# Kernel optimization log

Measured on AMD Instinct MI355X. Metric: run time of the kernel, lower is better.

## Reference

```python
import jax, jax.numpy as jnp
import numpy as np

VOCAB, H, B, L = 32000, 1024, 64, 256  # L leaves per complete binary tree


def setup_inputs() -> dict:
    key = jax.random.key(0)
    ks = jax.random.split(key, 12)
    s = 1.0 / np.sqrt(H)
    return {
        "tokens": jax.random.randint(ks[0], (B, L), 0, VOCAB),
        "emb":    jax.random.normal(ks[1], (VOCAB, H), jnp.float32) * 0.02,
        "W_iock": jax.random.normal(ks[2], (H, 3 * H), jnp.float32) * s,
        "b_iock": jax.random.normal(ks[3], (3 * H,), jnp.float32) * s,
        "U_iock": jax.random.normal(ks[4], (H, 3 * H), jnp.float32) * s,
        "W_fl":   jax.random.normal(ks[5], (H, H), jnp.float32) * s,
        "b_fl":   jax.random.normal(ks[6], (H,), jnp.float32) * s,
        "U_fl":   jax.random.normal(ks[7], (H, H), jnp.float32) * s,
        "W_fr":   jax.random.normal(ks[8], (H, H), jnp.float32) * s,
        "b_fr":   jax.random.normal(ks[9], (H,), jnp.float32) * s,
        "U_fr":   jax.random.normal(ks[10], (H, H), jnp.float32) * s,
    }


def _tree_lstm_levels(h, c, W_iock, b_iock, U_iock, W_fl, b_fl, U_fl, W_fr, b_fr, U_fr):
    """Bottom-up level sweep over a complete binary tree.

    h, c: (B, n, H) states of the current level. Each pass merges sibling
    pairs with the BinaryTreeLSTMCell.calculate gate math.
    """
    outs = []
    while h.shape[1] > 1:
        hl, hr = h[:, 0::2], h[:, 1::2]          # (B, n/2, H)
        cl, cr = c[:, 0::2], c[:, 1::2]
        # iock = W_iock(h_left) + U_iock(h_right); split -> i, o, c~
        iock = hl @ W_iock + hr @ U_iock + b_iock
        i_g, o_g, ck = jnp.split(iock, 3, axis=-1)
        fl = jax.nn.sigmoid(hl @ W_fl + hr @ U_fl + b_fl)
        fr = jax.nn.sigmoid(hl @ W_fr + hr @ U_fr + b_fr)
        c = jax.nn.sigmoid(i_g) * jnp.tanh(ck) + fl * cl + fr * cr
        h = jax.nn.sigmoid(o_g) * jnp.tanh(c)
        outs.append(h)
    forest_output = jnp.concatenate(outs, axis=1)  # (B, L-1, H) internal-node hiddens
    return forest_output, h, c


def reference(tokens, emb, W_iock, b_iock, U_iock, W_fl, b_fl, U_fl, W_fr, b_fr, U_fr):
    h = emb[tokens]                 # leaf hidden = embedding, (B, L, H)
    c = jnp.zeros_like(h)           # leaf memory cell = zeros
    forest_output, h_root, c_root = _tree_lstm_levels(
        h, c, W_iock, b_iock, U_iock, W_fl, b_fl, U_fl, W_fr, b_fr, U_fr)
    # (forest_output, (h, c)) with h, c as (1, B, H) like transpose(0, 1)
    return forest_output, (h_root.transpose(1, 0, 2), c_root.transpose(1, 0, 2))
```

## Files before the change

### kernel.cpp

```cpp
#include <hip/hip_runtime.h>
#include <stdint.h>

#define H     1024
#define K2    2048
#define NTOT  5120
#define BATCH 64
#define BM 128
#define BN 128
#define BK 64

typedef unsigned short u16;
typedef __attribute__((ext_vector_type(8))) short short8;
typedef __attribute__((ext_vector_type(4))) float floatx4;

__device__ __forceinline__ float bf2f(u16 u) {
    return __uint_as_float(((uint32_t)u) << 16);
}
__device__ __forceinline__ u16 f2bf(float f) {
    uint32_t u = __float_as_uint(f);
    u += 0x7fffu + ((u >> 16) & 1u);
    return (u16)(u >> 16);
}
__device__ __forceinline__ uint32_t pk2(float lo, float hi) {
    return (uint32_t)f2bf(lo) | ((uint32_t)f2bf(hi) << 16);
}
__device__ __forceinline__ float sigf(float x) {
    return 1.0f / (1.0f + __expf(-x));
}
__device__ __forceinline__ float tanh_(float x) {
    float e = __expf(-2.0f * fabsf(x));
    float r = (1.0f - e) / (1.0f + e);
    return copysignf(r, x);
}

__global__ void pack_weights(const float* __restrict__ Wio, const float* __restrict__ Uio,
                             const float* __restrict__ Wfl, const float* __restrict__ Ufl,
                             const float* __restrict__ Wfr, const float* __restrict__ Ufr,
                             u16* __restrict__ WT) {
    __shared__ u16 tile[32][33];
    int k0 = blockIdx.x * 32;
    int n0 = blockIdx.y * 32;
    const float *Wp, *Up; int ncols, nloc;
    if (n0 < 3072)      { Wp = Wio; Up = Uio; ncols = 3072; nloc = n0; }
    else if (n0 < 4096) { Wp = Wfl; Up = Ufl; ncols = 1024; nloc = n0 - 3072; }
    else                { Wp = Wfr; Up = Ufr; ncols = 1024; nloc = n0 - 4096; }
    int t = threadIdx.x;
    int c = t & 31, r = t >> 5;
#pragma unroll
    for (int i = 0; i < 4; ++i) {
        int rr = r + i * 8;
        int k = k0 + rr;
        float v = (k < 1024) ? Wp[(long)k * ncols + nloc + c]
                             : Up[(long)(k - 1024) * ncols + nloc + c];
        tile[rr][c] = f2bf(v);
    }
    __syncthreads();
#pragma unroll
    for (int i = 0; i < 4; ++i) {
        int rr = r + i * 8;
        WT[(long)(n0 + rr) * K2 + k0 + c] = tile[c][rr];
    }
}

__global__ void leaf_pack(const int* __restrict__ tokens, const float* __restrict__ emb,
                          u16* __restrict__ leaf) {
    int idx = blockIdx.x * 256 + threadIdx.x;
    int node = idx >> 8;
    int d4 = idx & 255;
    int tok = tokens[node];
    float4 v = ((const float4*)emb)[(long)tok * 256 + d4];
    uint2 o; o.x = pk2(v.x, v.y); o.y = pk2(v.z, v.w);
    ((uint2*)leaf)[(long)node * 256 + d4] = o;
}

__global__ void gemm_bt(const u16* __restrict__ A, const u16* __restrict__ BT,
                        float* __restrict__ G, int mc) {
    __shared__ __align__(16) u16 AsBs[16896];
    u16* As = AsBs;
    u16* Bs = AsBs + 8192;
    float* epi = (float*)AsBs;
    int tid  = threadIdx.x;
    int lane = tid & 63;
    int w    = tid >> 6;
    int wm   = w >> 1, wn = w & 1;
    int rowTile = blockIdx.x * BM;
    int n0      = blockIdx.y * BN;

    const u16* asrc[4];
    const u16* bsrc[4];
#pragma unroll
    for (int cc = 0; cc < 4; ++cc) {
        int r = cc * 32 + w * 8 + (lane >> 3);
        int j = rowTile + r; if (j >= mc) j = mc - 1;
        asrc[cc] = A + (long)j * K2 + (lane & 7) * 8;
        bsrc[cc] = BT + (long)(n0 + r) * K2 + (lane & 7) * 8;
    }

    floatx4 acc[4][4];
#pragma unroll
    for (int mt = 0; mt < 4; ++mt)
#pragma unroll
        for (int nt = 0; nt < 4; ++nt)
            acc[mt][nt] = (floatx4){0.f, 0.f, 0.f, 0.f};

    for (int k0 = 0; k0 < K2; k0 += BK) {
#pragma unroll
        for (int cc = 0; cc < 4; ++cc) {
            __builtin_amdgcn_global_load_lds(
                (const __attribute__((address_space(1))) void*)(asrc[cc] + k0),
                (__attribute__((address_space(3))) void*)(As + cc * 2048 + w * 512), 16, 0, 0);
            __builtin_amdgcn_global_load_lds(
                (const __attribute__((address_space(1))) void*)(bsrc[cc] + k0),
                (__attribute__((address_space(3))) void*)(Bs + cc * 2048 + w * 512), 16, 0, 0);
        }
        __syncthreads();
#pragma unroll
        for (int kb = 0; kb < 2; ++kb) {
            int kfo = kb * 32 + (lane >> 4) * 8;
            short8 af[4], bfv[4];
#pragma unroll
            for (int mt = 0; mt < 4; ++mt)
                af[mt] = *(const short8*)&As[(wm * 64 + mt * 16 + (lane & 15)) * BK + kfo];
#pragma unroll
            for (int nt = 0; nt < 4; ++nt)
                bfv[nt] = *(const short8*)&Bs[(wn * 64 + nt * 16 + (lane & 15)) * BK + kfo];
#pragma unroll
            for (int mt = 0; mt < 4; ++mt)
#pragma unroll
                for (int nt = 0; nt < 4; ++nt)
                    acc[mt][nt] = __builtin_amdgcn_mfma_f32_16x16x32_bf16(
                        af[mt], bfv[nt], acc[mt][nt], 0, 0, 0);
        }
        __syncthreads();
    }

#pragma unroll
    for (int s = 0; s < 2; ++s) {
        if (wm == s) {
#pragma unroll
            for (int mt = 0; mt < 4; ++mt)
#pragma unroll
                for (int r = 0; r < 4; ++r) {
                    int lrow = mt * 16 + (lane >> 4) * 4 + r;
#pragma unroll
                    for (int nt = 0; nt < 4; ++nt)
                        epi[lrow * 132 + wn * 64 + nt * 16 + (lane & 15)] = acc[mt][nt][r];
                }
        }
        __syncthreads();
        int gr0 = rowTile + s * 64;
#pragma unroll
        for (int k = 0; k < 8; ++k) {
            int f4 = tid + k * 256;
            int row = f4 >> 5, c4 = f4 & 31;
            if (gr0 + row < mc) {
                float4 v = *(const float4*)&epi[row * 132 + c4 * 4];
                *(float4*)&G[(long)(gr0 + row) * NTOT + n0 + c4 * 4] = v;
            }
        }
        __syncthreads();
    }
}

#define SWZ2(r) (((r) >> 1) & 3)

template <int BMW>
__global__ __launch_bounds__(512, 2) void gemmF(const u16* __restrict__ A,
                                                const u16* __restrict__ BT,
                                                const float* __restrict__ bio,
                                                const float* __restrict__ bfl,
                                                const float* __restrict__ bfr,
                                                const void* __restrict__ c_in,
                                                void* __restrict__ c_out, int c_bf16,
                                                float* __restrict__ outF,
                                                u16* __restrict__ hnext,
                                                int lp, int level_off, int gm) {
    constexpr int MF    = BMW / 64;
    constexpr int NA    = BMW / 64;
    constexpr int TOT   = NA + 5;
    constexpr int ABASE = (BMW / 128) * 8192;
    constexpr int BUFU  = ABASE + 20480;
    __shared__ __align__(16) u16 lds[2 * BUFU];
    const int tid  = threadIdx.x;
    const int lane = tid & 63;
    const int w    = tid >> 6;
    const int wm   = w >> 1;
    const int wd   = w & 1;

    int f = blockIdx.x;
    int xcd = f & 7, c = f >> 3;
    int by = (xcd & 1) * 8 + (c & 7);
    int bx = (xcd >> 1) * (gm >> 2) + (c >> 3);
    long rowTile = (long)bx * BMW;
    int d0 = by * 64;

    const u16* srcA[NA];
    {
        int rr_ = w * 16 + (lane >> 2);
        int ck_ = ((lane & 3) ^ SWZ2(rr_)) * 8;
#pragma unroll
        for (int cc = 0; cc < NA; ++cc)
            srcA[cc] = A + (rowTile + (cc >> 1) * 128 + rr_) * (long)K2 + (cc & 1) * 32 + ck_;
    }
    const u16* srcB[5];
    {
        int sr_ = (w >> 1) * 16 + (lane >> 2);
        int ck_ = ((lane & 3) ^ SWZ2(sr_)) * 8;
#pragma unroll
        for (int g = 0; g < 5; ++g)
            srcB[g] = BT + (long)(g * 1024 + d0 + sr_) * K2 + (w & 1) * 32 + ck_;
    }

    const int qv = lane >> 4;
    int rA[MF];
#pragma unroll
    for (int mf = 0; mf < MF; ++mf) {
        int rg = wm * (MF * 16) + mf * 16 + (lane & 15);
        int half = rg >> 7, rl = rg & 127;
        rA[mf] = half * 8192 + rl * 32 + ((qv ^ SWZ2(rl)) * 8);
    }
    int rB[2];
#pragma unroll
    for (int sub = 0; sub < 2; ++sub) {
        int rb = wd * 32 + sub * 16 + (lane & 15);
        rB[sub] = rb * 32 + ((qv ^ SWZ2(rb)) * 8);
    }

    floatx4 acc[MF][10];
#pragma unroll
    for (int mf = 0; mf < MF; ++mf)
#pragma unroll
        for (int nf = 0; nf < 10; ++nf)
            acc[mf][nf] = (floatx4){0.f, 0.f, 0.f, 0.f};

#define GF_STAGE_A(TT, DD)                                                           \
    do {                                                                             \
        _Pragma("unroll")                                                            \
        for (int cc = 0; cc < NA; ++cc)                                              \
            __builtin_amdgcn_global_load_lds(                                        \
                (const __attribute__((address_space(1))) void*)(srcA[cc] + (TT) * 64),\
                (__attribute__((address_space(3))) void*)(lds + (DD) * BUFU + (cc >> 1) * 8192 + (cc & 1) * 4096 + tid * 8), 16, 0, 0); \
    } while (0)

#define GF_STAGE_B(TT, DD, GG)                                                       \
    __builtin_amdgcn_global_load_lds(                                                \
        (const __attribute__((address_space(1))) void*)(srcB[GG] + (TT) * 64),       \
        (__attribute__((address_space(3))) void*)(lds + (DD) * BUFU + ABASE + (GG) * 4096 + (w & 1) * 2048 + (w >> 1) * 512 + lane * 8), 16, 0, 0)

#define GF_MFMA_G(GG)                                                                \
    do {                                                                             \
        __builtin_amdgcn_s_setprio(1);                                               \
        _Pragma("unroll")                                                            \
        for (int ks = 0; ks < 2; ++ks)                                               \
            _Pragma("unroll")                                                        \
            for (int mf = 0; mf < MF; ++mf)                                          \
                _Pragma("unroll")                                                    \
                for (int sub = 0; sub < 2; ++sub)                                    \
                    acc[mf][(GG) * 2 + sub] = __builtin_amdgcn_mfma_f32_16x16x32_bf16( \
                        aF[ks][mf], bF[ks][sub], acc[mf][(GG) * 2 + sub], 0, 0, 0);  \
        __builtin_amdgcn_s_setprio(0);                                               \
    } while (0)

    GF_STAGE_A(0, 0);
#pragma unroll
    for (int g = 0; g < 5; ++g) GF_STAGE_B(0, 0, g);

    short8 aF[2][MF], bF[2][2];
    for (int t = 0; t < 32; ++t) {
        int d = t & 1;
        const u16* bufD = lds + d * BUFU;
        bool last = (t == 31);
        asm volatile("s_waitcnt vmcnt(%0)" :: "i"(TOT - NA - 1) : "memory");
        asm volatile("s_barrier" ::: "memory");
#pragma unroll
        for (int ks = 0; ks < 2; ++ks) {
#pragma unroll
            for (int mf = 0; mf < MF; ++mf)
                aF[ks][mf] = *(const short8*)&bufD[rA[mf] + ks * 4096];
#pragma unroll
            for (int sub = 0; sub < 2; ++sub)
                bF[ks][sub] = *(const short8*)&bufD[ABASE + ks * 2048 + rB[sub]];
        }
        if (!last) GF_STAGE_A(t + 1, d ^ 1);
        GF_MFMA_G(0);
#pragma unroll
        for (int g = 1; g < 5; ++g) {
            if (!last) asm volatile("s_waitcnt vmcnt(%0)" :: "i"(TOT - 2) : "memory");
            else       asm volatile("s_waitcnt vmcnt(%0)" :: "i"(4 - g) : "memory");
            asm volatile("s_barrier" ::: "memory");
#pragma unroll
            for (int ks = 0; ks < 2; ++ks)
#pragma unroll
                for (int sub = 0; sub < 2; ++sub)
                    bF[ks][sub] = *(const short8*)&bufD[ABASE + g * 4096 + ks * 2048 + rB[sub]];
            if (!last) GF_STAGE_B(t + 1, d ^ 1, g - 1);
            GF_MFMA_G(g);
        }
        if (!last) GF_STAGE_B(t + 1, d ^ 1, 4);
    }
#undef GF_STAGE_A
#undef GF_STAGE_B
#undef GF_MFMA_G

    float bI[2], bO[2], bC[2], bL[2], bR[2];
    int dsub[2];
#pragma unroll
    for (int sub = 0; sub < 2; ++sub) {
        int dd = d0 + wd * 32 + sub * 16 + (lane & 15);
        dsub[sub] = dd;
        bI[sub] = bio[dd]; bO[sub] = bio[1024 + dd]; bC[sub] = bio[2048 + dd];
        bL[sub] = bfl[dd]; bR[sub] = bfr[dd];
    }
    int pmask = (1 << lp) - 1;
    int has_c = (c_in != nullptr);
#pragma unroll
    for (int mf = 0; mf < MF; ++mf) {
#pragma unroll
        for (int rr = 0; rr < 4; ++rr) {
            int row = wm * (MF * 16) + mf * 16 + (lane >> 4) * 4 + rr;
            long J = rowTile + row;
            int b = (int)(J >> lp), p = (int)(J & pmask);
            long ho = ((long)b * 255 + level_off + p) * H;
#pragma unroll
            for (int sub = 0; sub < 2; ++sub) {
                int dd = dsub[sub];
                float i_  = acc[mf][0 + sub][rr] + bI[sub];
                float o_  = acc[mf][2 + sub][rr] + bO[sub];
                float ck_ = acc[mf][4 + sub][rr] + bC[sub];
                float cv = sigf(i_) * tanh_(ck_);
                if (has_c) {
                    float fl_ = sigf(acc[mf][6 + sub][rr] + bL[sub]);
                    float fr_ = sigf(acc[mf][8 + sub][rr] + bR[sub]);
                    float cl, cr;
                    if (c_bf16) {
                        cl = bf2f(__builtin_nontemporal_load(
                                 (const u16*)c_in + (2 * J) * H + dd));
                        cr = bf2f(__builtin_nontemporal_load(
                                 (const u16*)c_in + (2 * J + 1) * H + dd));
                    } else {
                        cl = __builtin_nontemporal_load(
                                 (const float*)c_in + (2 * J) * H + dd);
                        cr = __builtin_nontemporal_load(
                                 (const float*)c_in + (2 * J + 1) * H + dd);
                    }
                    cv += fl_ * cl + fr_ * cr;
                }
                float hv = sigf(o_) * tanh_(cv);
                __builtin_nontemporal_store(hv, &outF[ho + dd]);
                if (c_bf16)
                    __builtin_nontemporal_store(f2bf(cv), (u16*)c_out + J * H + dd);
                else
                    __builtin_nontemporal_store(cv, (float*)c_out + J * H + dd);
                __builtin_nontemporal_store(f2bf(hv), hnext + J * H + dd);
            }
        }
    }
}

__global__ __launch_bounds__(512, 2) void gemmS(const u16* __restrict__ A,
                                                const u16* __restrict__ BT,
                                                float* __restrict__ P,
                                                int RT, int KS, int NT,
                                                int mLim, int mPad) {
    constexpr int ABASE = 8192;
    constexpr int BUFU  = 28672;
    __shared__ __align__(16) u16 lds[2 * BUFU];
    const int tid  = threadIdx.x;
    const int lane = tid & 63;
    const int w    = tid >> 6;
    const int wm   = w >> 1;
    const int wd   = w & 1;

    int nwg = RT * 16 * KS;
    int f = blockIdx.x;
    int q = nwg >> 3, r = nwg & 7;
    int xcd = f & 7, rank = f >> 3;
    int wg = (xcd < r ? xcd * (q + 1) : r * (q + 1) + (xcd - r) * q) + rank;
    int bx  = wg % RT;
    int by  = (wg / RT) % 16;
    int ksx = wg / (RT * 16);
    long rowTile = (long)bx * 128;
    int d0 = by * 64;
    int kOff = ksx * (NT * 64);

    const u16* srcA[2];
    {
        int rr_ = w * 16 + (lane >> 2);
        int ck_ = ((lane & 3) ^ SWZ2(rr_)) * 8;
#pragma unroll
        for (int c = 0; c < 2; ++c)
            srcA[c] = A + (rowTile + rr_) * (long)K2 + kOff + c * 32 + ck_;
    }
    const u16* srcB[5];
    {
        int sr_ = (w >> 1) * 16 + (lane >> 2);
        int ck_ = ((lane & 3) ^ SWZ2(sr_)) * 8;
#pragma unroll
        for (int g = 0; g < 5; ++g)
            srcB[g] = BT + (long)(g * 1024 + d0 + sr_) * K2 + kOff + (w & 1) * 32 + ck_;
    }

    const int qv = lane >> 4;
    int rA[2];
#pragma unroll
    for (int mf = 0; mf < 2; ++mf) {
        int rl = wm * 32 + mf * 16 + (lane & 15);
        rA[mf] = rl * 32 + ((qv ^ SWZ2(rl)) * 8);
    }
    int rB[2];
#pragma unroll
    for (int sub = 0; sub < 2; ++sub) {
        int rb = wd * 32 + sub * 16 + (lane & 15);
        rB[sub] = rb * 32 + ((qv ^ SWZ2(rb)) * 8);
    }

    floatx4 acc[2][10];
#pragma unroll
    for (int mf = 0; mf < 2; ++mf)
#pragma unroll
        for (int nf = 0; nf < 10; ++nf)
            acc[mf][nf] = (floatx4){0.f, 0.f, 0.f, 0.f};

#define GS_STAGE(TT, DD)                                                             \
    do {                                                                             \
        _Pragma("unroll")                                                            \
        for (int c = 0; c < 2; ++c)                                                  \
            __builtin_amdgcn_global_load_lds(                                        \
                (const __attribute__((address_space(1))) void*)(srcA[c] + (TT) * 64),\
                (__attribute__((address_space(3))) void*)(lds + (DD) * BUFU + c * 4096 + tid * 8), 16, 0, 0); \
        _Pragma("unroll")                                                            \
        for (int g = 0; g < 5; ++g)                                                  \
            __builtin_amdgcn_global_load_lds(                                        \
                (const __attribute__((address_space(1))) void*)(srcB[g] + (TT) * 64),\
                (__attribute__((address_space(3))) void*)(lds + (DD) * BUFU + ABASE + g * 4096 + (w & 1) * 2048 + (w >> 1) * 512 + lane * 8), 16, 0, 0); \
    } while (0)

    GS_STAGE(0, 0);

    for (int t = 0; t < NT; ++t) {
        int d = t & 1;
        asm volatile("s_barrier" ::: "memory");
        if (t < NT - 1) {
            GS_STAGE(t + 1, d ^ 1);
            asm volatile("s_waitcnt vmcnt(7)" ::: "memory");
        } else {
            asm volatile("s_waitcnt vmcnt(0)" ::: "memory");
        }
        asm volatile("s_barrier" ::: "memory");
        const u16* bufD = lds + d * BUFU;
#pragma unroll
        for (int ks = 0; ks < 2; ++ks) {
            short8 aF[2];
#pragma unroll
            for (int mf = 0; mf < 2; ++mf)
                aF[mf] = *(const short8*)&bufD[rA[mf] + ks * 4096];
#pragma unroll
            for (int g = 0; g < 5; ++g) {
                short8 bF[2];
#pragma unroll
                for (int sub = 0; sub < 2; ++sub)
                    bF[sub] = *(const short8*)&bufD[ABASE + g * 4096 + ks * 2048 + rB[sub]];
                __builtin_amdgcn_s_setprio(1);
#pragma unroll
                for (int mf = 0; mf < 2; ++mf)
#pragma unroll
                    for (int sub = 0; sub < 2; ++sub)
                        acc[mf][g * 2 + sub] = __builtin_amdgcn_mfma_f32_16x16x32_bf16(
                            aF[mf], bF[sub], acc[mf][g * 2 + sub], 0, 0, 0);
                __builtin_amdgcn_s_setprio(0);
            }
        }
    }
#undef GS_STAGE

    int dsub[2];
#pragma unroll
    for (int sub = 0; sub < 2; ++sub)
        dsub[sub] = d0 + wd * 32 + sub * 16 + (lane & 15);
#pragma unroll
    for (int mf = 0; mf < 2; ++mf) {
#pragma unroll
        for (int rr = 0; rr < 4; ++rr) {
            int row = wm * 32 + mf * 16 + (lane >> 4) * 4 + rr;
            long J = rowTile + row;
            if (J < mLim) {
                long pb = ((long)ksx * mPad + J) * NTOT;
#pragma unroll
                for (int g = 0; g < 5; ++g)
#pragma unroll
                    for (int sub = 0; sub < 2; ++sub)
                        P[pb + g * 1024 + dsub[sub]] = acc[mf][g * 2 + sub][rr];
            }
        }
    }
}

__global__ void redgate(const float* __restrict__ P, const float* __restrict__ bio,
                        const float* __restrict__ bfl, const float* __restrict__ bfr,
                        const void* __restrict__ c_in, void* __restrict__ c_out, int c_bf16,
                        float* __restrict__ outF, u16* __restrict__ hnext,
                        int lp, int level_off, int mc, int KS, int mPad) {
    int idx = blockIdx.x * 256 + threadIdx.x;
    int j = idx >> 8;
    if (j >= mc) return;
    int d = (idx & 255) * 4;
    int b = j >> lp, p = j & ((1 << lp) - 1);
    float ac[5][4] = {};
    for (int s = 0; s < KS; ++s) {
        long pb = ((long)s * mPad + j) * NTOT + d;
#pragma unroll
        for (int g = 0; g < 5; ++g) {
            float4 v = *(const float4*)&P[pb + g * 1024];
            ac[g][0] += v.x; ac[g][1] += v.y; ac[g][2] += v.z; ac[g][3] += v.w;
        }
    }
    float4 bi = *(const float4*)&bio[d];
    float4 bo = *(const float4*)&bio[1024 + d];
    float4 bc = *(const float4*)&bio[2048 + d];
    float4 bl = *(const float4*)&bfl[d];
    float4 br = *(const float4*)&bfr[d];
    const float* fbi = (const float*)&bi; const float* fbo = (const float*)&bo;
    const float* fbc = (const float*)&bc; const float* fbl = (const float*)&bl;
    const float* fbr = (const float*)&br;
    float clv[4], crv[4];
    {
        long cb = ((long)b * (2 << lp) + 2 * p) * H + d;
        if (c_bf16) {
            uint2 ul = *(const uint2*)((const u16*)c_in + cb);
            uint2 ur = *(const uint2*)((const u16*)c_in + cb + H);
            clv[0] = bf2f((u16)ul.x); clv[1] = bf2f((u16)(ul.x >> 16));
            clv[2] = bf2f((u16)ul.y); clv[3] = bf2f((u16)(ul.y >> 16));
            crv[0] = bf2f((u16)ur.x); crv[1] = bf2f((u16)(ur.x >> 16));
            crv[2] = bf2f((u16)ur.y); crv[3] = bf2f((u16)(ur.y >> 16));
        } else {
            float4 l4 = *(const float4*)((const float*)c_in + cb);
            float4 r4 = *(const float4*)((const float*)c_in + cb + H);
            clv[0] = l4.x; clv[1] = l4.y; clv[2] = l4.z; clv[3] = l4.w;
            crv[0] = r4.x; crv[1] = r4.y; crv[2] = r4.z; crv[3] = r4.w;
        }
    }
    float cv[4], hv[4];
#pragma unroll
    for (int qq = 0; qq < 4; ++qq) {
        float c = sigf(ac[0][qq] + fbi[qq]) * tanh_(ac[2][qq] + fbc[qq]);
        c += sigf(ac[3][qq] + fbl[qq]) * clv[qq] + sigf(ac[4][qq] + fbr[qq]) * crv[qq];
        cv[qq] = c;
        hv[qq] = sigf(ac[1][qq] + fbo[qq]) * tanh_(c);
    }
    long co = (long)j * H + d;
    if (c_bf16) {
        uint2 oc; oc.x = pk2(cv[0], cv[1]); oc.y = pk2(cv[2], cv[3]);
        *(uint2*)((u16*)c_out + co) = oc;
    } else {
        *(float4*)((float*)c_out + co) = make_float4(cv[0], cv[1], cv[2], cv[3]);
    }
    long oi = ((long)b * 255 + level_off + p) * H + d;
    *(float4*)&outF[oi] = make_float4(hv[0], hv[1], hv[2], hv[3]);
    uint2 oh; oh.x = pk2(hv[0], hv[1]); oh.y = pk2(hv[2], hv[3]);
    *(uint2*)(hnext + (long)j * H + d) = oh;
}

__global__ void gates(const float* __restrict__ G, const float* __restrict__ bio,
                      const float* __restrict__ bfl, const float* __restrict__ bfr,
                      const void* __restrict__ c_in, void* __restrict__ c_out, int c_bf16,
                      float* __restrict__ outF, u16* __restrict__ hnext,
                      int lp, int level_off, int row0, int mc) {
    int idx = blockIdx.x * 256 + threadIdx.x;
    int j = idx >> 8;
    if (j >= mc) return;
    int d = (idx & 255) * 4;
    int J = row0 + j;
    int b = J >> lp, p = J & ((1 << lp) - 1);
    long gb = (long)j * NTOT;
    float4 gi = *(const float4*)&G[gb + d];
    float4 go = *(const float4*)&G[gb + 1024 + d];
    float4 gc = *(const float4*)&G[gb + 2048 + d];
    float4 gl = *(const float4*)&G[gb + 3072 + d];
    float4 gr = *(const float4*)&G[gb + 4096 + d];
    float4 bi = *(const float4*)&bio[d];
    float4 bo = *(const float4*)&bio[1024 + d];
    float4 bc = *(const float4*)&bio[2048 + d];
    float4 bl = *(const float4*)&bfl[d];
    float4 br = *(const float4*)&bfr[d];
    float clv[4] = {0.f, 0.f, 0.f, 0.f}, crv[4] = {0.f, 0.f, 0.f, 0.f};
    if (c_in) {
        long cb = ((long)b * (2 << lp) + 2 * p) * H + d;
        if (c_bf16) {
            uint2 ul = *(const uint2*)((const u16*)c_in + cb);
            uint2 ur = *(const uint2*)((const u16*)c_in + cb + H);
            clv[0] = bf2f((u16)ul.x); clv[1] = bf2f((u16)(ul.x >> 16));
            clv[2] = bf2f((u16)ul.y); clv[3] = bf2f((u16)(ul.y >> 16));
            crv[0] = bf2f((u16)ur.x); crv[1] = bf2f((u16)(ur.x >> 16));
            crv[2] = bf2f((u16)ur.y); crv[3] = bf2f((u16)(ur.y >> 16));
        } else {
            float4 l4 = *(const float4*)((const float*)c_in + cb);
            float4 r4 = *(const float4*)((const float*)c_in + cb + H);
            clv[0] = l4.x; clv[1] = l4.y; clv[2] = l4.z; clv[3] = l4.w;
            crv[0] = r4.x; crv[1] = r4.y; crv[2] = r4.z; crv[3] = r4.w;
        }
    }
    const float* fgi = (const float*)&gi; const float* fgo = (const float*)&go;
    const float* fgc = (const float*)&gc; const float* fgl = (const float*)&gl;
    const float* fgr = (const float*)&gr;
    const float* fbi = (const float*)&bi; const float* fbo = (const float*)&bo;
    const float* fbc = (const float*)&bc; const float* fbl = (const float*)&bl;
    const float* fbr = (const float*)&br;
    float cv[4], hv[4];
    int has_c = (c_in != nullptr);
#pragma unroll
    for (int qq = 0; qq < 4; ++qq) {
        float c = sigf(fgi[qq] + fbi[qq]) * tanh_(fgc[qq] + fbc[qq]);
        if (has_c)
            c += sigf(fgl[qq] + fbl[qq]) * clv[qq] + sigf(fgr[qq] + fbr[qq]) * crv[qq];
        cv[qq] = c;
        hv[qq] = sigf(fgo[qq] + fbo[qq]) * tanh_(c);
    }
    long co = (long)J * H + d;
    if (c_bf16) {
        uint2 oc; oc.x = pk2(cv[0], cv[1]); oc.y = pk2(cv[2], cv[3]);
        *(uint2*)((u16*)c_out + co) = oc;
    } else {
        *(float4*)((float*)c_out + co) = make_float4(cv[0], cv[1], cv[2], cv[3]);
    }
    long oi = ((long)b * 255 + level_off + p) * H + d;
    *(float4*)&outF[oi] = make_float4(hv[0], hv[1], hv[2], hv[3]);
    uint2 oh; oh.x = pk2(hv[0], hv[1]); oh.y = pk2(hv[2], hv[3]);
    *(uint2*)(hnext + (long)J * H + d) = oh;
}

__global__ void root_copy(const float* __restrict__ outF, const void* __restrict__ c_root,
                          int c_bf16, float* __restrict__ tail) {
    int idx = blockIdx.x * 256 + threadIdx.x;
    if (idx < 65536) {
        int b = idx >> 10, d = idx & 1023;
        tail[idx] = outF[((long)b * 255 + 254) * H + d];
    } else {
        int i2 = idx - 65536;
        tail[idx] = c_bf16 ? bf2f(((const u16*)c_root)[i2]) : ((const float*)c_root)[i2];
    }
}

extern "C" void kernel_launch(void* const* d_in, const int* in_sizes, int n_in,
                              void* d_out, int out_size, void* d_ws, size_t ws_size,
                              hipStream_t stream) {
    const int* tokens = (const int*)d_in[0];
    const float* emb = (const float*)d_in[1];
    const float* Wio = (const float*)d_in[2];
    const float* bio = (const float*)d_in[3];
    const float* Uio = (const float*)d_in[4];
    const float* Wfl = (const float*)d_in[5];
    const float* bfl = (const float*)d_in[6];
    const float* Ufl = (const float*)d_in[7];
    const float* Wfr = (const float*)d_in[8];
    const float* bfr = (const float*)d_in[9];
    const float* Ufr = (const float*)d_in[10];
    float* outF = (float*)d_out;

    char* ws = (char*)d_ws;
    size_t off = 0;
    u16* WT   = (u16*)(ws + off); off += (size_t)NTOT * K2 * 2;
    u16* leaf = (u16*)(ws + off); off += (size_t)BATCH * 256 * H * 2;
    u16* hE   = (u16*)(ws + off); off += (size_t)8192 * H * 2;
    u16* hO   = (u16*)(ws + off); off += (size_t)4096 * H * 2;
    size_t cEf = (size_t)8192 * H, cOf = (size_t)4096 * H;
    int c_bf16 = (ws_size >= off + (cEf + cOf) * 4 + (size_t)512 * NTOT * 4) ? 0 : 1;
    size_t csz = c_bf16 ? 2 : 4;
    void* cE = (void*)(ws + off); off += cEf * csz;
    void* cO = (void*)(ws + off); off += cOf * csz;
    size_t avail = (ws_size > off) ? (ws_size - off) : 0;
    size_t Pbytes = (size_t)2048 * NTOT * 4;
    int splitOK = (avail >= Pbytes);
    float* P = (float*)(ws + off);
    long Grows = (long)(avail / ((size_t)NTOT * 4));
    if (Grows > 512) Grows = 512;
    Grows &= ~127L;
    if (Grows < 128) Grows = 128;
    float* G = (float*)(ws + off);

    pack_weights<<<dim3(64, 160), 256, 0, stream>>>(Wio, Uio, Wfl, Ufl, Wfr, Ufr, WT);
    leaf_pack<<<16384, 256, 0, stream>>>(tokens, emb, leaf);

    const int off_out[8] = {0, 128, 192, 224, 240, 248, 252, 254};
    for (int li = 0; li < 8; ++li) {
        int lp = 7 - li;
        long m = (long)BATCH << lp;
        const u16* Acur = (li == 0) ? leaf : ((li & 1) ? hE : hO);
        u16* hnext = (li & 1) ? hO : hE;
        const void* c_in = (li == 0) ? nullptr : ((li & 1) ? cE : cO);
        void* c_out = (li & 1) ? cO : cE;
        if (m >= 4096) {
            int gm = (int)(m >> 8);
            gemmF<256><<<gm * 16, 512, 0, stream>>>(Acur, WT, bio, bfl, bfr,
                                                    c_in, c_out, c_bf16, outF, hnext,
                                                    lp, off_out[li], gm);
        } else if (m >= 2048) {
            int gm = (int)(m >> 7);
            gemmF<128><<<gm * 16, 512, 0, stream>>>(Acur, WT, bio, bfl, bfr,
                                                    c_in, c_out, c_bf16, outF, hnext,
                                                    lp, off_out[li], gm);
        } else if (splitOK) {
            int KS = (m == 1024) ? 2 : (m == 512) ? 4 : (m == 256) ? 8 : 16;
            int RT = (m >= 128) ? (int)(m >> 7) : 1;
            int mPad = RT * 128;
            int NT = 32 / KS;
            gemmS<<<RT * 16 * KS, 512, 0, stream>>>(Acur, WT, P, RT, KS, NT,
                                                    (int)m, mPad);
            redgate<<<(int)m, 256, 0, stream>>>(P, bio, bfl, bfr, c_in, c_out, c_bf16,
                                                outF, hnext, lp, off_out[li],
                                                (int)m, KS, mPad);
        } else {
            for (long row0 = 0; row0 < m; row0 += Grows) {
                int mc = (int)((m - row0 > Grows) ? Grows : (m - row0));
                dim3 grid((mc + BM - 1) / BM, NTOT / BN);
                gemm_bt<<<grid, 256, 0, stream>>>(Acur + row0 * K2, WT, G, mc);
                gates<<<mc, 256, 0, stream>>>(G, bio, bfl, bfr, c_in, c_out, c_bf16,
                                              outF, hnext, lp, off_out[li], (int)row0, mc);
            }
        }
    }
    root_copy<<<512, 256, 0, stream>>>(outF, cO, c_bf16, outF + (size_t)BATCH * 255 * H);
}
```

Measured before the change: 661.3 us.

## Replace double-buffered fused GEMM with single-buffer rolling-stage 128-row kernel

The templated double-buffered gemmF kernel, which had 256- and 128-row variants, is replaced by gemmP128. The new kernel uses a single LDS buffer of about 56 KB. Loads for the next K-step are issued into slots as soon as those slots are consumed, and each stage ends with a combined vmcnt/lgkmcnt wait and barrier. Launch bounds rise to 4 blocks per SM, and the 256-row path for the largest levels is dropped so all m>=2048 levels use 128-row tiles. The aim is higher occupancy and less LDS per block, at the cost of more barriers, less reuse of B across rows, and tight ordering of loads within the buffer.

```diff
diff --git a/kernel.cpp b/kernel.cpp
--- a/kernel.cpp
+++ b/kernel.cpp
@@ -164,23 +164,20 @@
 
 #define SWZ2(r) (((r) >> 1) & 3)
 
-template <int BMW>
-__global__ __launch_bounds__(512, 2) void gemmF(const u16* __restrict__ A,
-                                                const u16* __restrict__ BT,
-                                                const float* __restrict__ bio,
-                                                const float* __restrict__ bfl,
-                                                const float* __restrict__ bfr,
-                                                const void* __restrict__ c_in,
-                                                void* __restrict__ c_out, int c_bf16,
-                                                float* __restrict__ outF,
-                                                u16* __restrict__ hnext,
-                                                int lp, int level_off, int gm) {
-    constexpr int MF    = BMW / 64;
-    constexpr int NA    = BMW / 64;
-    constexpr int TOT   = NA + 5;
-    constexpr int ABASE = (BMW / 128) * 8192;
-    constexpr int BUFU  = ABASE + 20480;
-    __shared__ __align__(16) u16 lds[2 * BUFU];
+#define GP_WAIT(VM)                                                                  \
+    asm volatile("s_waitcnt vmcnt(" #VM ") lgkmcnt(0)\n\ts_barrier" ::: "memory")
+
+__global__ __launch_bounds__(512, 4) void gemmP128(const u16* __restrict__ A,
+                                                   const u16* __restrict__ BT,
+                                                   const float* __restrict__ bio,
+                                                   const float* __restrict__ bfl,
+                                                   const float* __restrict__ bfr,
+                                                   const void* __restrict__ c_in,
+                                                   void* __restrict__ c_out, int c_bf16,
+                                                   float* __restrict__ outF,
+                                                   u16* __restrict__ hnext,
+                                                   int lp, int level_off, int gm) {
+    __shared__ __align__(16) u16 lds[28672];
     const int tid  = threadIdx.x;
     const int lane = tid & 63;
     const int w    = tid >> 6;
@@ -191,16 +188,16 @@
     int xcd = f & 7, c = f >> 3;
     int by = (xcd & 1) * 8 + (c & 7);
     int bx = (xcd >> 1) * (gm >> 2) + (c >> 3);
-    long rowTile = (long)bx * BMW;
+    long rowTile = (long)bx * 128;
     int d0 = by * 64;
 
-    const u16* srcA[NA];
+    const u16* srcA[2];
     {
         int rr_ = w * 16 + (lane >> 2);
         int ck_ = ((lane & 3) ^ SWZ2(rr_)) * 8;
 #pragma unroll
-        for (int cc = 0; cc < NA; ++cc)
-            srcA[cc] = A + (rowTile + (cc >> 1) * 128 + rr_) * (long)K2 + (cc & 1) * 32 + ck_;
+        for (int cc = 0; cc < 2; ++cc)
+            srcA[cc] = A + (rowTile + rr_) * (long)K2 + cc * 32 + ck_;
     }
     const u16* srcB[5];
     {
@@ -212,12 +209,11 @@
     }
 
     const int qv = lane >> 4;
-    int rA[MF];
-#pragma unroll
-    for (int mf = 0; mf < MF; ++mf) {
-        int rg = wm * (MF * 16) + mf * 16 + (lane & 15);
-        int half = rg >> 7, rl = rg & 127;
-        rA[mf] = half * 8192 + rl * 32 + ((qv ^ SWZ2(rl)) * 8);
+    int rA[2];
+#pragma unroll
+    for (int mf = 0; mf < 2; ++mf) {
+        int rg = wm * 32 + mf * 16 + (lane & 15);
+        rA[mf] = rg * 32 + ((qv ^ SWZ2(rg)) * 8);
     }
     int rB[2];
 #pragma unroll
@@ -226,34 +222,34 @@
         rB[sub] = rb * 32 + ((qv ^ SWZ2(rb)) * 8);
     }
 
-    floatx4 acc[MF][10];
-#pragma unroll
-    for (int mf = 0; mf < MF; ++mf)
+    floatx4 acc[2][10];
+#pragma unroll
+    for (int mf = 0; mf < 2; ++mf)
 #pragma unroll
         for (int nf = 0; nf < 10; ++nf)
             acc[mf][nf] = (floatx4){0.f, 0.f, 0.f, 0.f};
 
-#define GF_STAGE_A(TT, DD)                                                           \
+#define GP_STG_A(TT)                                                                 \
     do {                                                                             \
         _Pragma("unroll")                                                            \
-        for (int cc = 0; cc < NA; ++cc)                                              \
+        for (int cc = 0; cc < 2; ++cc)                                               \
             __builtin_amdgcn_global_load_lds(                                        \
                 (const __attribute__((address_space(1))) void*)(srcA[cc] + (TT) * 64),\
-                (__attribute__((address_space(3))) void*)(lds + (DD) * BUFU + (cc >> 1) * 8192 + (cc & 1) * 4096 + tid * 8), 16, 0, 0); \
+                (__attribute__((address_space(3))) void*)(lds + cc * 4096 + tid * 8), 16, 0, 0); \
     } while (0)
 
-#define GF_STAGE_B(TT, DD, GG)                                                       \
+#define GP_STG_B(TT, GG)                                                             \
     __builtin_amdgcn_global_load_lds(                                                \
         (const __attribute__((address_space(1))) void*)(srcB[GG] + (TT) * 64),       \
-        (__attribute__((address_space(3))) void*)(lds + (DD) * BUFU + ABASE + (GG) * 4096 + (w & 1) * 2048 + (w >> 1) * 512 + lane * 8), 16, 0, 0)
-
-#define GF_MFMA_G(GG)                                                                \
+        (__attribute__((address_space(3))) void*)(lds + 8192 + (GG) * 4096 + (w & 1) * 2048 + (w >> 1) * 512 + lane * 8), 16, 0, 0)
+
+#define GP_MFMA(GG)                                                                  \
     do {                                                                             \
         __builtin_amdgcn_s_setprio(1);                                               \
         _Pragma("unroll")                                                            \
         for (int ks = 0; ks < 2; ++ks)                                               \
             _Pragma("unroll")                                                        \
-            for (int mf = 0; mf < MF; ++mf)                                          \
+            for (int mf = 0; mf < 2; ++mf)                                           \
                 _Pragma("unroll")                                                    \
                 for (int sub = 0; sub < 2; ++sub)                                    \
                     acc[mf][(GG) * 2 + sub] = __builtin_amdgcn_mfma_f32_16x16x32_bf16( \
@@ -261,46 +257,77 @@
         __builtin_amdgcn_s_setprio(0);                                               \
     } while (0)
 
-    GF_STAGE_A(0, 0);
-#pragma unroll
-    for (int g = 0; g < 5; ++g) GF_STAGE_B(0, 0, g);
-
-    short8 aF[2][MF], bF[2][2];
-    for (int t = 0; t < 32; ++t) {
-        int d = t & 1;
-        const u16* bufD = lds + d * BUFU;
-        bool last = (t == 31);
-        asm volatile("s_waitcnt vmcnt(%0)" :: "i"(TOT - NA - 1) : "memory");
-        asm volatile("s_barrier" ::: "memory");
-#pragma unroll
-        for (int ks = 0; ks < 2; ++ks) {
-#pragma unroll
-            for (int mf = 0; mf < MF; ++mf)
-                aF[ks][mf] = *(const short8*)&bufD[rA[mf] + ks * 4096];
-#pragma unroll
-            for (int sub = 0; sub < 2; ++sub)
-                bF[ks][sub] = *(const short8*)&bufD[ABASE + ks * 2048 + rB[sub]];
-        }
-        if (!last) GF_STAGE_A(t + 1, d ^ 1);
-        GF_MFMA_G(0);
-#pragma unroll
-        for (int g = 1; g < 5; ++g) {
-            if (!last) asm volatile("s_waitcnt vmcnt(%0)" :: "i"(TOT - 2) : "memory");
-            else       asm volatile("s_waitcnt vmcnt(%0)" :: "i"(4 - g) : "memory");
-            asm volatile("s_barrier" ::: "memory");
-#pragma unroll
-            for (int ks = 0; ks < 2; ++ks)
-#pragma unroll
-                for (int sub = 0; sub < 2; ++sub)
-                    bF[ks][sub] = *(const short8*)&bufD[ABASE + g * 4096 + ks * 2048 + rB[sub]];
-            if (!last) GF_STAGE_B(t + 1, d ^ 1, g - 1);
-            GF_MFMA_G(g);
-        }
-        if (!last) GF_STAGE_B(t + 1, d ^ 1, 4);
-    }
-#undef GF_STAGE_A
-#undef GF_STAGE_B
-#undef GF_MFMA_G
+#define GP_READ_A_B0()                                                               \
+    do {                                                                             \
+        _Pragma("unroll")                                                            \
+        for (int ks = 0; ks < 2; ++ks) {                                             \
+            _Pragma("unroll")                                                        \
+            for (int mf = 0; mf < 2; ++mf)                                           \
+                aF[ks][mf] = *(const short8*)&lds[rA[mf] + ks * 4096];               \
+            _Pragma("unroll")                                                        \
+            for (int sub = 0; sub < 2; ++sub)                                        \
+                bF[ks][sub] = *(const short8*)&lds[8192 + ks * 2048 + rB[sub]];      \
+        }                                                                            \
+    } while (0)
+
+#define GP_READ_B(GG)                                                                \
+    do {                                                                             \
+        _Pragma("unroll")                                                            \
+        for (int ks = 0; ks < 2; ++ks)                                               \
+            _Pragma("unroll")                                                        \
+            for (int sub = 0; sub < 2; ++sub)                                        \
+                bF[ks][sub] = *(const short8*)&lds[8192 + (GG) * 4096 + ks * 2048 + rB[sub]]; \
+    } while (0)
+
+    GP_STG_A(0);
+    GP_STG_B(0, 0); GP_STG_B(0, 1); GP_STG_B(0, 2); GP_STG_B(0, 3);
+
+    short8 aF[2][2], bF[2][2];
+    for (int t = 0; t < 31; ++t) {
+        GP_WAIT(3);
+        GP_READ_A_B0();
+        GP_STG_B(t, 4);
+        GP_MFMA(0);
+        GP_WAIT(3);
+        GP_READ_B(1);
+        GP_STG_A(t + 1);
+        GP_MFMA(1);
+        GP_WAIT(4);
+        GP_READ_B(2);
+        GP_STG_B(t + 1, 0);
+        GP_MFMA(2);
+        GP_WAIT(4);
+        GP_READ_B(3);
+        GP_STG_B(t + 1, 1);
+        GP_MFMA(3);
+        GP_WAIT(4);
+        GP_READ_B(4);
+        GP_STG_B(t + 1, 2);
+        GP_STG_B(t + 1, 3);
+        GP_MFMA(4);
+    }
+    GP_WAIT(3);
+    GP_READ_A_B0();
+    GP_STG_B(31, 4);
+    GP_MFMA(0);
+    GP_WAIT(3);
+    GP_READ_B(1);
+    GP_MFMA(1);
+    GP_WAIT(2);
+    GP_READ_B(2);
+    GP_MFMA(2);
+    GP_WAIT(1);
+    GP_READ_B(3);
+    GP_MFMA(3);
+    GP_WAIT(0);
+    GP_READ_B(4);
+    GP_MFMA(4);
+
+#undef GP_STG_A
+#undef GP_STG_B
+#undef GP_MFMA
+#undef GP_READ_A_B0
+#undef GP_READ_B
 
     float bI[2], bO[2], bC[2], bL[2], bR[2];
     int dsub[2];
@@ -314,10 +341,10 @@
     int pmask = (1 << lp) - 1;
     int has_c = (c_in != nullptr);
 #pragma unroll
-    for (int mf = 0; mf < MF; ++mf) {
+    for (int mf = 0; mf < 2; ++mf) {
 #pragma unroll
         for (int rr = 0; rr < 4; ++rr) {
-            int row = wm * (MF * 16) + mf * 16 + (lane >> 4) * 4 + rr;
+            int row = wm * 32 + mf * 16 + (lane >> 4) * 4 + rr;
             long J = rowTile + row;
             int b = (int)(J >> lp), p = (int)(J & pmask);
             long ho = ((long)b * 255 + level_off + p) * H;
@@ -688,16 +715,11 @@
         u16* hnext = (li & 1) ? hO : hE;
         const void* c_in = (li == 0) ? nullptr : ((li & 1) ? cE : cO);
         void* c_out = (li & 1) ? cO : cE;
-        if (m >= 4096) {
-            int gm = (int)(m >> 8);
-            gemmF<256><<<gm * 16, 512, 0, stream>>>(Acur, WT, bio, bfl, bfr,
-                                                    c_in, c_out, c_bf16, outF, hnext,
-                                                    lp, off_out[li], gm);
-        } else if (m >= 2048) {
+        if (m >= 2048) {
             int gm = (int)(m >> 7);
-            gemmF<128><<<gm * 16, 512, 0, stream>>>(Acur, WT, bio, bfl, bfr,
-                                                    c_in, c_out, c_bf16, outF, hnext,
-                                                    lp, off_out[li], gm);
+            gemmP128<<<gm * 16, 512, 0, stream>>>(Acur, WT, bio, bfl, bfr,
+                                                  c_in, c_out, c_bf16, outF, hnext,
+                                                  lp, off_out[li], gm);
         } else if (splitOK) {
             int KS = (m == 1024) ? 2 : (m == 512) ? 4 : (m == 256) ? 8 : 16;
             int RT = (m >= 128) ? (int)(m >> 7) : 1;
```

Result: no change. 674.4 us (+2.0%).
